# Performance work log

Hardware: AMD Instinct MI355X
Metric: run time of the kernel (lower is better)

The kernel has to match this reference:

```python
import jax, jax.numpy as jnp
import numpy as np

N, E, F_IN, H, OUT = 50000, 1600000, 128, 128, 32
NEG_SLOPE = 0.2


def setup_inputs() -> dict:
    key = jax.random.key(0)
    ks = jax.random.split(key, 9)
    s = lambda fan: 1.0 / np.sqrt(fan)
    x = jax.random.normal(ks[0], (N, F_IN), jnp.float32)
    edge_index = jax.random.randint(ks[1], (2, E), 0, N, jnp.int64)
    Wl1 = jax.random.normal(ks[2], (F_IN, H), jnp.float32) * s(F_IN)
    Wr1 = jax.random.normal(ks[3], (F_IN, H), jnp.float32) * s(F_IN)
    att1 = jax.random.normal(ks[4], (H,), jnp.float32) * s(H)
    b1 = jnp.zeros((H,), jnp.float32)
    Wl2 = jax.random.normal(ks[5], (H, OUT), jnp.float32) * s(H)
    Wr2 = jax.random.normal(ks[6], (H, OUT), jnp.float32) * s(H)
    att2 = jax.random.normal(ks[7], (OUT,), jnp.float32) * s(OUT)
    b2 = jnp.zeros((OUT,), jnp.float32)
    return {"x": x, "edge_index": edge_index, "Wl1": Wl1, "Wr1": Wr1,
            "att1": att1, "b1": b1, "Wl2": Wl2, "Wr2": Wr2, "att2": att2, "b2": b2}


def gatv2_layer(x, Wl, Wr, att, bias, src, dst, num_nodes):
    # PyG GATv2Conv (heads=1, concat=True, add_self_loops handled by caller)
    xl = x @ Wl  # source-side transform  [N, C]
    xr = x @ Wr  # target-side transform  [N, C]
    e = jax.nn.leaky_relu(xl[src] + xr[dst], NEG_SLOPE)  # [E, C]
    logits = e @ att  # [E]
    # segment softmax over incoming edges of each destination node
    m = jax.ops.segment_max(logits, dst, num_segments=num_nodes)  # [N]
    expv = jnp.exp(logits - m[dst])
    denom = jax.ops.segment_sum(expv, dst, num_segments=num_nodes)  # [N]
    alpha = expv / (denom[dst] + 1e-16)  # [E]
    out = jax.ops.segment_sum(xl[src] * alpha[:, None], dst, num_segments=num_nodes)
    return out + bias


def reference(x, edge_index, Wl1, Wr1, att1, b1, Wl2, Wr2, att2, b2):
    # add self-loops (PyG add_self_loops=True default)
    loops = jnp.arange(N, dtype=edge_index.dtype)
    src = jnp.concatenate([edge_index[0], loops])
    dst = jnp.concatenate([edge_index[1], loops])
    h = gatv2_layer(x, Wl1, Wr1, att1, b1, src, dst, N)
    h = jax.nn.relu(h)
    h = gatv2_layer(h, Wl2, Wr2, att2, b2, src, dst, N)
    return jax.nn.relu(h)
```

## Files before the change

### kernel.cpp

```cpp
#include <hip/hip_runtime.h>
#include <hip/hip_bf16.h>

#define N_NODES 50000
#define E_EDGES 1600000
#define E_TOT   (E_EDGES + N_NODES)
#define NEG_SLOPE 0.2f

#define NB       196
#define S1_TILE  4096
#define NT       ((E_TOT + S1_TILE - 1) / S1_TILE)
#define S2_CAP   12288

typedef _Float16 h2 __attribute__((ext_vector_type(2)));
typedef _Float16 h4 __attribute__((ext_vector_type(4)));
typedef _Float16 h8 __attribute__((ext_vector_type(8)));

__device__ __forceinline__ float fdot2h(h2 a, h2 b, float c)
{
#if __has_builtin(__builtin_amdgcn_fdot2)
    return __builtin_amdgcn_fdot2(a, b, c, false);
#else
    return c + (float)a[0] * (float)b[0] + (float)a[1] * (float)b[1];
#endif
}

__device__ __forceinline__ h2 habs2(h2 e)
{
    unsigned int u = __builtin_bit_cast(unsigned int, e) & 0x7FFF7FFFu;
    return __builtin_bit_cast(h2, u);
}

__device__ __forceinline__ int wave_iscan(int v, int lane)
{
#pragma unroll
    for (int off = 1; off < 64; off <<= 1) {
        int u = __shfl_up(v, off);
        if (lane >= off) v += u;
    }
    return v;
}

__global__ __launch_bounds__(256) void transform1_gemm(
    const float* __restrict__ x,
    const float* __restrict__ Wl, const float* __restrict__ Wr,
    _Float16* __restrict__ xl, _Float16* __restrict__ xr)
{
    __shared__ h2 xs2[16][128];
    __shared__ h2 ws2[16][128];
    const int n0 = blockIdx.x * 128;
    const float* __restrict__ W = blockIdx.y ? Wr : Wl;
    _Float16* __restrict__ Y = blockIdx.y ? xr : xl;
    const int t = threadIdx.x;
    const int tc = t & 15;
    const int tn = t >> 4;

    float acc[2][4][2][4];
#pragma unroll
    for (int nh = 0; nh < 2; ++nh)
#pragma unroll
        for (int i = 0; i < 4; ++i)
#pragma unroll
            for (int ch = 0; ch < 2; ++ch)
#pragma unroll
                for (int j = 0; j < 4; ++j) acc[nh][i][ch][j] = 0.f;

    for (int k0 = 0; k0 < 128; k0 += 32) {
        {
            const int node = t >> 1;
            const int kh = (t & 1) * 16;
            const int gn = n0 + node;
#pragma unroll
            for (int q = 0; q < 4; ++q) {
                float4 v = make_float4(0.f, 0.f, 0.f, 0.f);
                if (gn < N_NODES)
                    v = *(const float4*)&x[(size_t)gn * 128 + k0 + kh + q * 4];
                h2 p0 = {(_Float16)v.x, (_Float16)v.y};
                h2 p1 = {(_Float16)v.z, (_Float16)v.w};
                xs2[kh / 2 + q * 2 + 0][node] = p0;
                xs2[kh / 2 + q * 2 + 1][node] = p1;
            }
        }
        {
            const int c = t & 127;
            const int kq = (t >> 7) * 16;
#pragma unroll
            for (int ii = 0; ii < 8; ++ii) {
                h2 pw = {(_Float16)W[(size_t)(k0 + kq + 2 * ii) * 128 + c],
                         (_Float16)W[(size_t)(k0 + kq + 2 * ii + 1) * 128 + c]};
                ws2[kq / 2 + ii][c] = pw;
            }
        }
        __syncthreads();
#pragma unroll 4
        for (int k2 = 0; k2 < 16; ++k2) {
            h2 a0[4], a1[4], b0[4], b1[4];
#pragma unroll
            for (int j = 0; j < 4; ++j) {
                a0[j] = xs2[k2][tn * 4 + j];
                a1[j] = xs2[k2][64 + tn * 4 + j];
                b0[j] = ws2[k2][tc * 4 + j];
                b1[j] = ws2[k2][64 + tc * 4 + j];
            }
#pragma unroll
            for (int i = 0; i < 4; ++i)
#pragma unroll
                for (int j = 0; j < 4; ++j) {
                    acc[0][i][0][j] = fdot2h(a0[i], b0[j], acc[0][i][0][j]);
                    acc[0][i][1][j] = fdot2h(a0[i], b1[j], acc[0][i][1][j]);
                    acc[1][i][0][j] = fdot2h(a1[i], b0[j], acc[1][i][0][j]);
                    acc[1][i][1][j] = fdot2h(a1[i], b1[j], acc[1][i][1][j]);
                }
        }
        __syncthreads();
    }
#pragma unroll
    for (int nh = 0; nh < 2; ++nh)
#pragma unroll
        for (int i = 0; i < 4; ++i) {
            const int node = n0 + nh * 64 + tn * 4 + i;
            if (node < N_NODES) {
#pragma unroll
                for (int ch = 0; ch < 2; ++ch) {
                    h4 v;
                    v[0] = (_Float16)acc[nh][i][ch][0];
                    v[1] = (_Float16)acc[nh][i][ch][1];
                    v[2] = (_Float16)acc[nh][i][ch][2];
                    v[3] = (_Float16)acc[nh][i][ch][3];
                    *(h4*)&Y[(size_t)node * 128 + ch * 64 + tc * 4] = v;
                }
            }
        }
}

__global__ __launch_bounds__(256) void transform2_gemm(
    const _Float16* __restrict__ h,
    const float* __restrict__ Wl, const float* __restrict__ Wr,
    _Float16* __restrict__ hl, _Float16* __restrict__ hr)
{
    __shared__ h2 xs2[16][128];
    __shared__ h2 ws2[16][64];
    const int n0 = blockIdx.x * 128;
    const int t = threadIdx.x;
    const int tc = t & 15;
    const int tn = t >> 4;

    float acc[2][4][4];
#pragma unroll
    for (int nh = 0; nh < 2; ++nh)
#pragma unroll
        for (int i = 0; i < 4; ++i)
#pragma unroll
            for (int j = 0; j < 4; ++j) acc[nh][i][j] = 0.f;

    for (int k0 = 0; k0 < 128; k0 += 32) {
        {
            const int node = t >> 1;
            const int kh = (t & 1) * 16;
            const int gn = n0 + node;
            h8 v0 = {}, v1 = {};
            if (gn < N_NODES) {
                v0 = *(const h8*)&h[(size_t)gn * 128 + k0 + kh];
                v1 = *(const h8*)&h[(size_t)gn * 128 + k0 + kh + 8];
            }
#pragma unroll
            for (int q = 0; q < 4; ++q) {
                h2 p0 = {v0[2 * q], v0[2 * q + 1]};
                h2 p1 = {v1[2 * q], v1[2 * q + 1]};
                xs2[kh / 2 + q][node] = p0;
                xs2[kh / 2 + 4 + q][node] = p1;
            }
        }
        {
            const int c = t & 63;
            const int kq = (t >> 6) * 8;
            const float* __restrict__ Wm = (c < 32) ? Wl : Wr;
            const int wc = c & 31;
#pragma unroll
            for (int ii = 0; ii < 4; ++ii) {
                h2 pw = {(_Float16)Wm[(size_t)(k0 + kq + 2 * ii) * 32 + wc],
                         (_Float16)Wm[(size_t)(k0 + kq + 2 * ii + 1) * 32 + wc]};
                ws2[kq / 2 + ii][c] = pw;
            }
        }
        __syncthreads();
#pragma unroll 4
        for (int k2 = 0; k2 < 16; ++k2) {
            h2 a0[4], a1[4], b[4];
#pragma unroll
            for (int j = 0; j < 4; ++j) {
                a0[j] = xs2[k2][tn * 4 + j];
                a1[j] = xs2[k2][64 + tn * 4 + j];
                b[j] = ws2[k2][tc * 4 + j];
            }
#pragma unroll
            for (int i = 0; i < 4; ++i)
#pragma unroll
                for (int j = 0; j < 4; ++j) {
                    acc[0][i][j] = fdot2h(a0[i], b[j], acc[0][i][j]);
                    acc[1][i][j] = fdot2h(a1[i], b[j], acc[1][i][j]);
                }
        }
        __syncthreads();
    }
    _Float16* __restrict__ Y = (tc < 8) ? hl : hr;
    const int col = (tc < 8) ? tc * 4 : tc * 4 - 32;
#pragma unroll
    for (int nh = 0; nh < 2; ++nh)
#pragma unroll
        for (int i = 0; i < 4; ++i) {
            const int node = n0 + nh * 64 + tn * 4 + i;
            if (node < N_NODES) {
                h4 v;
                v[0] = (_Float16)acc[nh][i][0];
                v[1] = (_Float16)acc[nh][i][1];
                v[2] = (_Float16)acc[nh][i][2];
                v[3] = (_Float16)acc[nh][i][3];
                *(h4*)&Y[(size_t)node * 32 + col] = v;
            }
        }
}

__global__ __launch_bounds__(512) void tile_hist(
    const int* __restrict__ src, const int* __restrict__ dst,
    int* __restrict__ counts)
{
    __shared__ int hh[NB];
    const int t = threadIdx.x;
    const int base = blockIdx.x * S1_TILE;
    for (int i = t; i < NB; i += 512) hh[i] = 0;
    __syncthreads();
#pragma unroll
    for (int k = 0; k < S1_TILE / 512; ++k) {
        const int i = base + k * 512 + t;
        if (i < E_TOT) {
            const int d = (i < E_EDGES) ? dst[i] : (i - E_EDGES);
            atomicAdd(&hh[d >> 8], 1);
        }
    }
    __syncthreads();
    for (int b = t; b < NB; b += 512)
        counts[blockIdx.x * NB + b] = hh[b];
}

__global__ __launch_bounds__(512) void row_scan(
    const int* __restrict__ counts, int* __restrict__ rstart,
    int* __restrict__ bcount)
{
    __shared__ int wsum[8];
    const int b = blockIdx.x;
    const int t = threadIdx.x;
    const int lane = t & 63, wid = t >> 6;
    const int v = (t < NT) ? counts[t * NB + b] : 0;
    int inc = wave_iscan(v, lane);
    if (lane == 63) wsum[wid] = inc;
    __syncthreads();
    if (t == 0) {
        int s = 0;
#pragma unroll
        for (int w = 0; w < 8; ++w) { int u = wsum[w]; wsum[w] = s; s += u; }
    }
    __syncthreads();
    const int excl = inc - v + wsum[wid];
    if (t < NT) rstart[b * NT + t] = excl;
    if (t == 511) bcount[b] = excl;
}

__global__ __launch_bounds__(256) void bucket_base(
    const int* __restrict__ bcount, int* __restrict__ bbase)
{
    __shared__ int wsum[4];
    const int t = threadIdx.x;
    const int lane = t & 63, wid = t >> 6;
    int v = (t < NB) ? bcount[t] : 0;
    int inc = wave_iscan(v, lane);
    if (lane == 63) wsum[wid] = inc;
    __syncthreads();
    if (t == 0) {
        int s = 0;
#pragma unroll
        for (int w = 0; w < 4; ++w) { int u = wsum[w]; wsum[w] = s; s += u; }
    }
    __syncthreads();
    const int excl = inc - v + wsum[wid];
    if (t < NB) bbase[t] = excl;
    if (t == NB - 1) bbase[NB] = excl + v;
}

__global__ __launch_bounds__(512) void tile_scatter(
    const int* __restrict__ src, const int* __restrict__ dst,
    const int* __restrict__ rstart, const int* __restrict__ bbase,
    unsigned int* __restrict__ bucket_data)
{
    __shared__ int hh[256];
    __shared__ int cur[NB];
    __shared__ int rs[NB];
    __shared__ int wsum[8];
    __shared__ unsigned int srt[S1_TILE];
    const int t = threadIdx.x;
    const int tile = blockIdx.x;
    const int base = tile * S1_TILE;
    const int tcount = min(S1_TILE, E_TOT - base);

    for (int i = t; i < 256; i += 512) hh[i] = 0;
    __syncthreads();

    int eb[S1_TILE / 512];
    unsigned int ee[S1_TILE / 512];
#pragma unroll
    for (int k = 0; k < S1_TILE / 512; ++k) {
        const int i = base + k * 512 + t;
        eb[k] = -1;
        if (i < E_TOT) {
            int s, d;
            if (i < E_EDGES) { s = src[i]; d = dst[i]; }
            else { s = i - E_EDGES; d = s; }
            const int b = d >> 8;
            eb[k] = b;
            ee[k] = ((unsigned)b << 24) | ((unsigned)(d & 255) << 16) | (unsigned)s;
            atomicAdd(&hh[b], 1);
        }
    }
    __syncthreads();
    {
        const int lane = t & 63, wid = t >> 6;
        const int v = (t < 256) ? hh[t] : 0;
        int inc = wave_iscan(v, lane);
        if (lane == 63 && wid < 4) wsum[wid] = inc;
        __syncthreads();
        if (t == 0) {
            int s = 0;
#pragma unroll
            for (int w = 0; w < 4; ++w) { int u = wsum[w]; wsum[w] = s; s += u; }
        }
        __syncthreads();
        if (t < NB) {
            const int excl = inc - v + wsum[wid];
            cur[t] = excl;
            rs[t] = bbase[t] + rstart[t * NT + tile] - excl;
        }
    }
    __syncthreads();
#pragma unroll
    for (int k = 0; k < S1_TILE / 512; ++k) {
        if (eb[k] >= 0) {
            const int pos = atomicAdd(&cur[eb[k]], 1);
            srt[pos] = ee[k];
        }
    }
    __syncthreads();
    for (int i = t; i < tcount; i += 512) {
        const unsigned int e = srt[i];
        bucket_data[rs[e >> 24] + i] = e;
    }
}

__global__ __launch_bounds__(1024) void bucket_sort(
    const unsigned int* __restrict__ bucket_data,
    const int* __restrict__ bbase,
    int* __restrict__ offs, unsigned short* __restrict__ sorted_src)
{
    __shared__ int hist[256];
    __shared__ int cur[256];
    __shared__ int wsum[4];
    __shared__ unsigned short srt[S2_CAP];
    const int b = blockIdx.x;
    const int t = threadIdx.x;
    const int lo = bbase[b], hi = bbase[b + 1];
    const int c = hi - lo;
    if (t < 256) hist[t] = 0;
    __syncthreads();
    for (int i = t; i < c; i += 1024)
        atomicAdd(&hist[(bucket_data[lo + i] >> 16) & 255u], 1);
    __syncthreads();
    {
        const int lane = t & 63, wid = t >> 6;
        const int v = (t < 256) ? hist[t] : 0;
        int inc = wave_iscan(v, lane);
        if (lane == 63 && wid < 4) wsum[wid] = inc;
        __syncthreads();
        if (t == 0) {
            int s = 0;
#pragma unroll
            for (int w = 0; w < 4; ++w) { int u = wsum[w]; wsum[w] = s; s += u; }
        }
        __syncthreads();
        if (t < 256) {
            const int excl = inc - v + wsum[wid];
            cur[t] = excl;
            const int node = b * 256 + t;
            if (node < N_NODES) offs[node] = lo + excl;
        }
    }
    if (b == 0 && t == 0) offs[N_NODES] = E_TOT;
    __syncthreads();
    for (int i = t; i < c; i += 1024) {
        const unsigned int e = bucket_data[lo + i];
        const int pos = atomicAdd(&cur[(e >> 16) & 255u], 1);
        srt[pos] = (unsigned short)(e & 0xFFFFu);
    }
    __syncthreads();
    for (int i = t; i < c; i += 1024)
        sorted_src[lo + i] = srt[i];
}

template <int C, int LPG, typename OUT_T>
__global__ __launch_bounds__(256) void gat_edge_pass(
    const _Float16* __restrict__ xl, const _Float16* __restrict__ xr,
    const float* __restrict__ att, const float* __restrict__ bias,
    const int* __restrict__ offs, const unsigned short* __restrict__ ssrc,
    OUT_T* __restrict__ out)
{
    constexpr int GPB = 256 / LPG;
    static_assert(C == LPG * 8, "8 halves per lane");
    const int node = blockIdx.x * GPB + threadIdx.x / LPG;
    if (node >= N_NODES) return;
    const int lane = threadIdx.x % LPG;
    const int cb = lane * 8;

    h2 a6[4], a4[4], r2[4];
    {
        const h8 rv = *(const h8*)(xr + (size_t)node * C + cb);
#pragma unroll
        for (int i = 0; i < 4; ++i) {
            const float av0 = att[cb + 2 * i], av1 = att[cb + 2 * i + 1];
            h2 t6 = {(_Float16)(0.6f * av0), (_Float16)(0.6f * av1)};
            h2 t4 = {(_Float16)(0.4f * av0), (_Float16)(0.4f * av1)};
            a6[i] = t6; a4[i] = t4;
            h2 rr = {rv[2 * i], rv[2 * i + 1]};
            r2[i] = rr;
        }
    }
    float acc[8];
#pragma unroll
    for (int v = 0; v < 8; ++v) acc[v] = 0.f;
    float m = -3.0e38f, denom = 0.f;

    const int pB = offs[node];
    const int p1 = offs[node + 1];
    int p = pB;
    const int nq = (p1 - pB) >> 2;

    h8 x0, x1, x2, x3;
    int i0 = 0, i1 = 0, i2 = 0, i3 = 0;
    if (nq > 0) {
        const int s0 = ssrc[p], s1 = ssrc[p + 1];
        const int s2 = ssrc[p + 2], s3 = ssrc[p + 3];
        x0 = *(const h8*)(xl + (size_t)s0 * C + cb);
        x1 = *(const h8*)(xl + (size_t)s1 * C + cb);
        x2 = *(const h8*)(xl + (size_t)s2 * C + cb);
        x3 = *(const h8*)(xl + (size_t)s3 * C + cb);
    }
    if (nq > 1) {
        i0 = ssrc[p + 4]; i1 = ssrc[p + 5];
        i2 = ssrc[p + 6]; i3 = ssrc[p + 7];
    }

    for (int q = 0; q < nq; ++q) {
        const bool more  = (q + 1 < nq);
        const bool more2 = (q + 2 < nq);
        int j0 = 0, j1 = 0, j2 = 0, j3 = 0;
        if (more2) {
            j0 = ssrc[p + 8];  j1 = ssrc[p + 9];
            j2 = ssrc[p + 10]; j3 = ssrc[p + 11];
        }
        h8 y0 = {}, y1 = {}, y2 = {}, y3 = {};
        if (more) {
            y0 = *(const h8*)(xl + (size_t)i0 * C + cb);
            y1 = *(const h8*)(xl + (size_t)i1 * C + cb);
            y2 = *(const h8*)(xl + (size_t)i2 * C + cb);
            y3 = *(const h8*)(xl + (size_t)i3 * C + cb);
        }
        float d0 = 0.f, d1 = 0.f, d2 = 0.f, d3 = 0.f;
#pragma unroll
        for (int i = 0; i < 4; ++i) {
            h2 xa = {x0[2 * i], x0[2 * i + 1]};
            h2 xb = {x1[2 * i], x1[2 * i + 1]};
            h2 xc = {x2[2 * i], x2[2 * i + 1]};
            h2 xd = {x3[2 * i], x3[2 * i + 1]};
            h2 e0 = xa + r2[i], e1 = xb + r2[i];
            h2 e2 = xc + r2[i], e3 = xd + r2[i];
            d0 = fdot2h(a6[i], e0, fdot2h(a4[i], habs2(e0), d0));
            d1 = fdot2h(a6[i], e1, fdot2h(a4[i], habs2(e1), d1));
            d2 = fdot2h(a6[i], e2, fdot2h(a4[i], habs2(e2), d2));
            d3 = fdot2h(a6[i], e3, fdot2h(a4[i], habs2(e3), d3));
        }
#pragma unroll
        for (int off = LPG >> 1; off; off >>= 1) {
            d0 += __shfl_xor(d0, off);
            d1 += __shfl_xor(d1, off);
            d2 += __shfl_xor(d2, off);
            d3 += __shfl_xor(d3, off);
        }
        const float pm = fmaxf(fmaxf(d0, d1), fmaxf(d2, d3));
        if (__builtin_expect(pm > m + 8.f, 0)) {
            const float sc = __expf(m - pm);
            m = pm;
            denom *= sc;
#pragma unroll
            for (int v = 0; v < 8; ++v) acc[v] *= sc;
        }
        const float w0 = __expf(d0 - m), w1 = __expf(d1 - m);
        const float w2 = __expf(d2 - m), w3 = __expf(d3 - m);
        denom += (w0 + w1) + (w2 + w3);
        const h2 wA = {(_Float16)w0, (_Float16)w1};
        const h2 wB = {(_Float16)w2, (_Float16)w3};
#pragma unroll
        for (int v = 0; v < 8; ++v) {
            h2 pA = {x0[v], x1[v]};
            h2 pB = {x2[v], x3[v]};
            acc[v] = fdot2h(wA, pA, fdot2h(wB, pB, acc[v]));
        }
        if (more)  { x0 = y0; x1 = y1; x2 = y2; x3 = y3; }
        if (more2) { i0 = j0; i1 = j1; i2 = j2; i3 = j3; }
        p += 4;
    }
    for (; p < p1; ++p) {
        const int s0 = ssrc[p];
        const h8 t0 = *(const h8*)(xl + (size_t)s0 * C + cb);
        float d0 = 0.f;
#pragma unroll
        for (int i = 0; i < 4; ++i) {
            h2 xa = {t0[2 * i], t0[2 * i + 1]};
            h2 e0 = xa + r2[i];
            d0 = fdot2h(a6[i], e0, fdot2h(a4[i], habs2(e0), d0));
        }
#pragma unroll
        for (int off = LPG >> 1; off; off >>= 1) d0 += __shfl_xor(d0, off);
        if (d0 > m + 8.f) {
            const float sc = __expf(m - d0);
            m = d0;
            denom *= sc;
#pragma unroll
            for (int v = 0; v < 8; ++v) acc[v] *= sc;
        }
        const float w0 = __expf(d0 - m);
        denom += w0;
        const h2 wA = {(_Float16)w0, (_Float16)0.f};
#pragma unroll
        for (int v = 0; v < 8; ++v) {
            h2 pA = {t0[v], t0[v]};
            acc[v] = fdot2h(wA, pA, acc[v]);
        }
    }

    const float inv = 1.f / (denom + 1e-16f);
    if constexpr (sizeof(OUT_T) == 2) {
        h8 o;
#pragma unroll
        for (int v = 0; v < 8; ++v)
            o[v] = (_Float16)fmaxf(fmaf(acc[v], inv, bias[cb + v]), 0.f);
        *(h8*)&out[(size_t)node * C + cb] = o;
    } else {
        float4 o0, o1;
        o0.x = fmaxf(fmaf(acc[0], inv, bias[cb + 0]), 0.f);
        o0.y = fmaxf(fmaf(acc[1], inv, bias[cb + 1]), 0.f);
        o0.z = fmaxf(fmaf(acc[2], inv, bias[cb + 2]), 0.f);
        o0.w = fmaxf(fmaf(acc[3], inv, bias[cb + 3]), 0.f);
        o1.x = fmaxf(fmaf(acc[4], inv, bias[cb + 4]), 0.f);
        o1.y = fmaxf(fmaf(acc[5], inv, bias[cb + 5]), 0.f);
        o1.z = fmaxf(fmaf(acc[6], inv, bias[cb + 6]), 0.f);
        o1.w = fmaxf(fmaf(acc[7], inv, bias[cb + 7]), 0.f);
        *(float4*)&out[(size_t)node * C + cb] = o0;
        *(float4*)&out[(size_t)node * C + cb + 4] = o1;
    }
}

extern "C" void kernel_launch(void* const* d_in, const int* in_sizes, int n_in,
                              void* d_out, int out_size, void* d_ws, size_t ws_size,
                              hipStream_t stream)
{
    const float* x    = (const float*)d_in[0];
    const int*   ei   = (const int*)d_in[1];
    const float* Wl1  = (const float*)d_in[2];
    const float* Wr1  = (const float*)d_in[3];
    const float* att1 = (const float*)d_in[4];
    const float* b1   = (const float*)d_in[5];
    const float* Wl2  = (const float*)d_in[6];
    const float* Wr2  = (const float*)d_in[7];
    const float* att2 = (const float*)d_in[8];
    const float* b2   = (const float*)d_in[9];
    float* out = (float*)d_out;

    const int* e_src = ei;
    const int* e_dst = ei + E_EDGES;

    char* ws = (char*)d_ws;
    _Float16* xl = (_Float16*)(ws + 0);
    _Float16* xr = (_Float16*)(ws + 25600000);
    _Float16* h  = (_Float16*)(ws + 51200000);
    unsigned short* sorted_src = (unsigned short*)(ws + 76800000);
    int* offs   = (int*)(ws + 83400192);
    int* bbase  = (int*)(ws + 83600384);
    int* bcount = (int*)(ws + 83602432);
    unsigned int* bucket_data = (unsigned int*)(ws + 51200000);
    int* counts = (int*)(ws + 58000000);
    int* rstart = (int*)(ws + 58400000);
    _Float16* hl = xl;
    _Float16* hr = xr;

    transform1_gemm<<<dim3((N_NODES + 127) / 128, 2), 256, 0, stream>>>(
        x, Wl1, Wr1, xl, xr);

    tile_hist<<<NT, 512, 0, stream>>>(e_src, e_dst, counts);
    row_scan<<<NB, 512, 0, stream>>>(counts, rstart, bcount);
    bucket_base<<<1, 256, 0, stream>>>(bcount, bbase);
    tile_scatter<<<NT, 512, 0, stream>>>(e_src, e_dst, rstart, bbase, bucket_data);
    bucket_sort<<<NB, 1024, 0, stream>>>(bucket_data, bbase, offs, sorted_src);

    gat_edge_pass<128, 16, _Float16><<<N_NODES * 16 / 256, 256, 0, stream>>>(
        xl, xr, att1, b1, offs, sorted_src, h);

    transform2_gemm<<<(N_NODES + 127) / 128, 256, 0, stream>>>(
        h, Wl2, Wr2, hl, hr);

    gat_edge_pass<32, 4, float><<<(N_NODES * 4 + 255) / 256, 256, 0, stream>>>(
        hl, hr, att2, b2, offs, sorted_src, out);
}
```

Baseline: 186.7 us.

## Pre-sort bucket edges by source bits; simplify edge loop with 2-edge tail

The bucket sort now runs a second counting pass on bits 8-15 of the packed edge word before the destination-key scatter. Because the scatter is stable, edges inside each destination end up ordered by source index, which is meant to make xl gathers more cache-local. The edge pass drops the software-pipelined prefetch of the next four rows and indices in favour of a plain 4-edge loop plus a new 2-edge and 1-edge tail, cutting register pressure at the cost of exposed load latency. The shared-memory capacity shrinks to fit a 32-bit staging buffer alongside the 16-bit one, which lowers the maximum bucket size the sort can hold.

```diff
diff --git a/kernel.cpp b/kernel.cpp
--- a/kernel.cpp
+++ b/kernel.cpp
@@ -9,7 +9,7 @@
 #define NB       196
 #define S1_TILE  4096
 #define NT       ((E_TOT + S1_TILE - 1) / S1_TILE)
-#define S2_CAP   12288
+#define S2_CAP   10240
 
 typedef _Float16 h2 __attribute__((ext_vector_type(2)));
 typedef _Float16 h4 __attribute__((ext_vector_type(4)));
@@ -360,18 +360,39 @@
     int* __restrict__ offs, unsigned short* __restrict__ sorted_src)
 {
     __shared__ int hist[256];
+    __shared__ int hsrc[256];
     __shared__ int cur[256];
+    __shared__ int csrc[256];
     __shared__ int wsum[4];
-    __shared__ unsigned short srt[S2_CAP];
+    __shared__ unsigned int srt4[S2_CAP];
+    __shared__ unsigned short srt2[S2_CAP];
     const int b = blockIdx.x;
     const int t = threadIdx.x;
     const int lo = bbase[b], hi = bbase[b + 1];
     const int c = hi - lo;
-    if (t < 256) hist[t] = 0;
-    __syncthreads();
-    for (int i = t; i < c; i += 1024)
-        atomicAdd(&hist[(bucket_data[lo + i] >> 16) & 255u], 1);
-    __syncthreads();
+    if (t < 256) { hist[t] = 0; hsrc[t] = 0; }
+    __syncthreads();
+    for (int i = t; i < c; i += 1024) {
+        const unsigned int e = bucket_data[lo + i];
+        atomicAdd(&hist[(e >> 16) & 255u], 1);
+        atomicAdd(&hsrc[(e >> 8) & 255u], 1);
+    }
+    __syncthreads();
+    {
+        const int lane = t & 63, wid = t >> 6;
+        const int v = (t < 256) ? hsrc[t] : 0;
+        int inc = wave_iscan(v, lane);
+        if (lane == 63 && wid < 4) wsum[wid] = inc;
+        __syncthreads();
+        if (t == 0) {
+            int s = 0;
+#pragma unroll
+            for (int w = 0; w < 4; ++w) { int u = wsum[w]; wsum[w] = s; s += u; }
+        }
+        __syncthreads();
+        if (t < 256) csrc[t] = inc - v + wsum[wid];
+        __syncthreads();
+    }
     {
         const int lane = t & 63, wid = t >> 6;
         const int v = (t < 256) ? hist[t] : 0;
@@ -395,12 +416,18 @@
     __syncthreads();
     for (int i = t; i < c; i += 1024) {
         const unsigned int e = bucket_data[lo + i];
+        const int pos = atomicAdd(&csrc[(e >> 8) & 255u], 1);
+        srt4[pos] = e;
+    }
+    __syncthreads();
+    for (int i = t; i < c; i += 1024) {
+        const unsigned int e = srt4[i];
         const int pos = atomicAdd(&cur[(e >> 16) & 255u], 1);
-        srt[pos] = (unsigned short)(e & 0xFFFFu);
+        srt2[pos] = (unsigned short)(e & 0xFFFFu);
     }
     __syncthreads();
     for (int i = t; i < c; i += 1024)
-        sorted_src[lo + i] = srt[i];
+        sorted_src[lo + i] = srt2[i];
 }
 
 template <int C, int LPG, typename OUT_T>
@@ -435,41 +462,16 @@
     for (int v = 0; v < 8; ++v) acc[v] = 0.f;
     float m = -3.0e38f, denom = 0.f;
 
-    const int pB = offs[node];
     const int p1 = offs[node + 1];
-    int p = pB;
-    const int nq = (p1 - pB) >> 2;
-
-    h8 x0, x1, x2, x3;
-    int i0 = 0, i1 = 0, i2 = 0, i3 = 0;
-    if (nq > 0) {
+    int p = offs[node];
+
+    for (; p + 4 <= p1; p += 4) {
         const int s0 = ssrc[p], s1 = ssrc[p + 1];
         const int s2 = ssrc[p + 2], s3 = ssrc[p + 3];
-        x0 = *(const h8*)(xl + (size_t)s0 * C + cb);
-        x1 = *(const h8*)(xl + (size_t)s1 * C + cb);
-        x2 = *(const h8*)(xl + (size_t)s2 * C + cb);
-        x3 = *(const h8*)(xl + (size_t)s3 * C + cb);
-    }
-    if (nq > 1) {
-        i0 = ssrc[p + 4]; i1 = ssrc[p + 5];
-        i2 = ssrc[p + 6]; i3 = ssrc[p + 7];
-    }
-
-    for (int q = 0; q < nq; ++q) {
-        const bool more  = (q + 1 < nq);
-        const bool more2 = (q + 2 < nq);
-        int j0 = 0, j1 = 0, j2 = 0, j3 = 0;
-        if (more2) {
-            j0 = ssrc[p + 8];  j1 = ssrc[p + 9];
-            j2 = ssrc[p + 10]; j3 = ssrc[p + 11];
-        }
-        h8 y0 = {}, y1 = {}, y2 = {}, y3 = {};
-        if (more) {
-            y0 = *(const h8*)(xl + (size_t)i0 * C + cb);
-            y1 = *(const h8*)(xl + (size_t)i1 * C + cb);
-            y2 = *(const h8*)(xl + (size_t)i2 * C + cb);
-            y3 = *(const h8*)(xl + (size_t)i3 * C + cb);
-        }
+        const h8 x0 = *(const h8*)(xl + (size_t)s0 * C + cb);
+        const h8 x1 = *(const h8*)(xl + (size_t)s1 * C + cb);
+        const h8 x2 = *(const h8*)(xl + (size_t)s2 * C + cb);
+        const h8 x3 = *(const h8*)(xl + (size_t)s3 * C + cb);
         float d0 = 0.f, d1 = 0.f, d2 = 0.f, d3 = 0.f;
 #pragma unroll
         for (int i = 0; i < 4; ++i) {
@@ -510,17 +512,49 @@
             h2 pB = {x2[v], x3[v]};
             acc[v] = fdot2h(wA, pA, fdot2h(wB, pB, acc[v]));
         }
-        if (more)  { x0 = y0; x1 = y1; x2 = y2; x3 = y3; }
-        if (more2) { i0 = j0; i1 = j1; i2 = j2; i3 = j3; }
-        p += 4;
-    }
-    for (; p < p1; ++p) {
+    }
+    for (; p + 2 <= p1; p += 2) {
+        const int s0 = ssrc[p], s1 = ssrc[p + 1];
+        const h8 x0 = *(const h8*)(xl + (size_t)s0 * C + cb);
+        const h8 x1 = *(const h8*)(xl + (size_t)s1 * C + cb);
+        float d0 = 0.f, d1 = 0.f;
+#pragma unroll
+        for (int i = 0; i < 4; ++i) {
+            h2 xa = {x0[2 * i], x0[2 * i + 1]};
+            h2 xb = {x1[2 * i], x1[2 * i + 1]};
+            h2 e0 = xa + r2[i], e1 = xb + r2[i];
+            d0 = fdot2h(a6[i], e0, fdot2h(a4[i], habs2(e0), d0));
+            d1 = fdot2h(a6[i], e1, fdot2h(a4[i], habs2(e1), d1));
+        }
+#pragma unroll
+        for (int off = LPG >> 1; off; off >>= 1) {
+            d0 += __shfl_xor(d0, off);
+            d1 += __shfl_xor(d1, off);
+        }
+        const float pm = fmaxf(d0, d1);
+        if (__builtin_expect(pm > m + 8.f, 0)) {
+            const float sc = __expf(m - pm);
+            m = pm;
+            denom *= sc;
+#pragma unroll
+            for (int v = 0; v < 8; ++v) acc[v] *= sc;
+        }
+        const float w0 = __expf(d0 - m), w1 = __expf(d1 - m);
+        denom += w0 + w1;
+        const h2 wA = {(_Float16)w0, (_Float16)w1};
+#pragma unroll
+        for (int v = 0; v < 8; ++v) {
+            h2 pA = {x0[v], x1[v]};
+            acc[v] = fdot2h(wA, pA, acc[v]);
+        }
+    }
+    if (p < p1) {
         const int s0 = ssrc[p];
-        const h8 t0 = *(const h8*)(xl + (size_t)s0 * C + cb);
+        const h8 x0 = *(const h8*)(xl + (size_t)s0 * C + cb);
         float d0 = 0.f;
 #pragma unroll
         for (int i = 0; i < 4; ++i) {
-            h2 xa = {t0[2 * i], t0[2 * i + 1]};
+            h2 xa = {x0[2 * i], x0[2 * i + 1]};
             h2 e0 = xa + r2[i];
             d0 = fdot2h(a6[i], e0, fdot2h(a4[i], habs2(e0), d0));
         }
@@ -538,7 +572,7 @@
         const h2 wA = {(_Float16)w0, (_Float16)0.f};
 #pragma unroll
         for (int v = 0; v < 8; ++v) {
-            h2 pA = {t0[v], t0[v]};
+            h2 pA = {x0[v], x0[v]};
             acc[v] = fdot2h(wA, pA, acc[v]);
         }
     }
```

Measured after the change: 166.5 us. -10.8%, faster.
